# Performance work log

Measured on AMD Instinct MI355X. Metric: run time of the kernel, lower is better.

The kernel has to match this reference:

```python
import jax, jax.numpy as jnp
import numpy as np

EPS = 1e-6

def rms_norm(x):
    # RMSNorm over last dim, no learned weight (torch F.rms_norm without weight)
    return x * jax.lax.rsqrt(jnp.mean(jnp.square(x), axis=-1, keepdims=True) + EPS)

def apply_rotary_emb(x, cos, sin):
    # x: [b, t, h, d]; cos/sin: [t, d//2] -> broadcast [1, t, 1, d//2]
    half = x.shape[-1] // 2
    c = cos[None, :, None, :]
    s = sin[None, :, None, :]
    x1, x2 = x[..., :half], x[..., half:]
    return jnp.concatenate([x1 * c - x2 * s, x2 * c + x1 * s], axis=-1)

def setup_inputs() -> dict:
    key = jax.random.key(0)
    ks = jax.random.split(key, 16)
    B, T, E, H = 4, 2048, 1024, 16
    D = E // H
    inp = {
        "query": jax.random.normal(ks[0], (B, T, E), jnp.float32),
        "key": jax.random.normal(ks[1], (B, T, E), jnp.float32),
        "value": jax.random.normal(ks[2], (B, T, E), jnp.float32),
        "attn_mask": jnp.tril(jnp.ones((T, T), dtype=bool)),
        "cos": jnp.cos(jnp.arange(T)[:, None] / (10000.0 ** (jnp.arange(D // 2) / (D // 2)))[None, :]).astype(jnp.float32),
        "sin": jnp.sin(jnp.arange(T)[:, None] / (10000.0 ** (jnp.arange(D // 2) / (D // 2)))[None, :]).astype(jnp.float32),
        "Wq": jax.random.normal(ks[3], (E, E), jnp.float32) * 0.02,
        "bq": jnp.zeros((E,), jnp.float32),
        "Wk": jax.random.normal(ks[4], (E, E), jnp.float32) * 0.02,
        "bk": jnp.zeros((E,), jnp.float32),
        "Wv": jax.random.normal(ks[5], (E, E), jnp.float32) * 0.02,
        "bv": jnp.zeros((E,), jnp.float32),
        "Wo": jax.random.normal(ks[6], (E, E), jnp.float32) * 0.02,
        "bo": jnp.zeros((E,), jnp.float32),
    }
    return inp

def reference(query, key, value, attn_mask, cos, sin, Wq, bq, Wk, bk, Wv, bv, Wo, bo):
    B, T, E = query.shape
    H = 16
    D = E // H
    q = query @ Wq.T + bq
    k = key @ Wk.T + bk
    v = value @ Wv.T + bv
    q = q.reshape(B, T, H, D)
    k = k.reshape(B, T, H, D)
    v = v.reshape(B, T, H, D)
    q, k = rms_norm(q), rms_norm(k)
    q = apply_rotary_emb(q, cos, sin)
    k = apply_rotary_emb(k, cos, sin)
    # SDPA: [b, h, t, d] layout via einsum directly from [b, t, h, d]
    scale = 1.0 / jnp.sqrt(jnp.float32(D))
    scores = jnp.einsum('bqhd,bkhd->bhqk', q, k) * scale
    scores = jnp.where(attn_mask[None, None, :, :], scores, jnp.float32(-jnp.inf))
    attn = jax.nn.softmax(scores, axis=-1)
    o = jnp.einsum('bhqk,bkhd->bqhd', attn, v).reshape(B, T, E)
    return o @ Wo.T + bo
```

## Files before the change

### kernel.cpp

```cpp
#include <hip/hip_runtime.h>

typedef __bf16 bf16;
typedef __bf16 bf16x8 __attribute__((ext_vector_type(8)));
typedef __bf16 bf16x4 __attribute__((ext_vector_type(4)));
typedef float  floatx4 __attribute__((ext_vector_type(4)));

#define B_ 4
#define T_ 2048
#define E_ 1024
#define H_ 16
#define D_ 64
#define NTE_ (B_ * T_ * E_)

#define NEG_BIG (-1e30f)
#define SMAX2 12.2629081f

#define OFF_CQ 0ull
#define OFF_CK ((unsigned long long)NTE_)
#define OFF_CV (2ull * NTE_)
#define OFF_WQ (3ull * NTE_)
#define OFF_WK (OFF_WQ + 1048576ull)
#define OFF_WV (OFF_WK + 1048576ull)
#define OFF_WO (OFF_WV + 1048576ull)
__device__ bf16 g_conv[3ull * NTE_ + 4ull * 1048576ull];
__device__ bf16 g_scratch[5ull * NTE_];

__device__ __forceinline__ floatx4 mfma16(bf16x8 a, bf16x8 b, floatx4 c) {
  return __builtin_amdgcn_mfma_f32_16x16x32_bf16(a, b, c, 0, 0, 0);
}

__device__ __forceinline__ void async_copy16(void* lds, const void* g) {
  __builtin_amdgcn_global_load_lds(
      (const __attribute__((address_space(1))) unsigned int*)g,
      (__attribute__((address_space(3))) unsigned int*)lds, 16, 0, 0);
}

__global__ __launch_bounds__(256) void convert_all(const float4* __restrict__ q,
                                                   const float4* __restrict__ k,
                                                   const float4* __restrict__ v,
                                                   const float4* __restrict__ wq,
                                                   const float4* __restrict__ wk,
                                                   const float4* __restrict__ wv,
                                                   const float4* __restrict__ wo) {
  const float4* srcs[7] = {q, k, v, wq, wk, wv, wo};
  bf16x4* dsts[7] = {(bf16x4*)(g_conv + OFF_CQ), (bf16x4*)(g_conv + OFF_CK),
                     (bf16x4*)(g_conv + OFF_CV), (bf16x4*)(g_conv + OFF_WQ),
                     (bf16x4*)(g_conv + OFF_WK), (bf16x4*)(g_conv + OFF_WV),
                     (bf16x4*)(g_conv + OFF_WO)};
  const int n4s[7] = {NTE_ / 4, NTE_ / 4, NTE_ / 4, 262144, 262144, 262144, 262144};
  int i0 = blockIdx.x * 256 + threadIdx.x;
  int stride = gridDim.x * 256;
#pragma unroll
  for (int s = 0; s < 7; ++s) {
    const float4* sp = srcs[s];
    bf16x4* dp = dsts[s];
    int n4 = n4s[s];
    for (int i = i0; i < n4; i += stride) {
      float4 vv = sp[i];
      bf16x4 o;
      o[0] = (bf16)vv.x; o[1] = (bf16)vv.y; o[2] = (bf16)vv.z; o[3] = (bf16)vv.w;
      dp[i] = o;
    }
  }
}

template <int EPI>
__device__ __forceinline__ void gemm_core(char* __restrict__ smem,
                                          const bf16* __restrict__ X,
                                          const bf16* __restrict__ W,
                                          const float* __restrict__ bias,
                                          void* __restrict__ Yv, int M0, int N0,
                                          const float* __restrict__ cosb,
                                          const float* __restrict__ sinb) {
  constexpr int NT = 16;

  const int tid = threadIdx.x;
  const int w = tid >> 6;
  const int l = tid & 63;
  const int q = l >> 4;
  const int r = l & 15;
  const int lrow = l >> 3;
  const int rs7 = r & 7;
  const int wm = (w >> 2) * 64;
  const int wn = (w & 3) * 64;
  const int colb = ((l & 7) ^ lrow) << 4;
  const int sl0 = ((0 + q) ^ rs7) << 4;
  const int sl1 = ((4 + q) ^ rs7) << 4;

  char* const Ab = smem;
  char* const Bb = smem + 32768;
  const int aoff = (wm + r) * 128;
  const int boff = (wn + r) * 128;

  const char* gA = (const char*)X + (size_t)(M0 + w * 16 + lrow) * 2048 + colb;
  const char* gB = (const char*)W + (size_t)(N0 + w * 32 + lrow) * 2048 + colb;

  floatx4 acc[4][4];
#pragma unroll
  for (int mi = 0; mi < 4; ++mi)
#pragma unroll
    for (int ni = 0; ni < 4; ++ni) acc[mi][ni] = (floatx4){0.f, 0.f, 0.f, 0.f};

#define STA(p, t)                                              \
  do {                                                         \
    char* d_ = Ab + (p) * 16384 + w * 2048;                    \
    const char* s_ = gA + (size_t)(t) * 128;                   \
    async_copy16(d_, s_);                                      \
    async_copy16(d_ + 1024, s_ + 16384);                       \
  } while (0)
#define STB(p, t)                                              \
  do {                                                         \
    char* d_ = Bb + (p) * 32768 + w * 4096;                    \
    const char* s_ = gB + (size_t)(t) * 128;                   \
    async_copy16(d_, s_);                                      \
    async_copy16(d_ + 1024, s_ + 16384);                       \
    async_copy16(d_ + 2048, s_ + 32768);                       \
    async_copy16(d_ + 3072, s_ + 49152);                       \
  } while (0)

  STB(0, 0); STA(0, 0);
  STB(1, 1); STA(1, 1);
  asm volatile("s_waitcnt vmcnt(6)" ::: "memory");
  __builtin_amdgcn_s_barrier();

  bf16x8 af[4][2], bf0[2][2], bf1[2][2];

#pragma unroll 2
  for (int t = 0; t < NT; ++t) {
    const int p = t & 1;
    const char* rA = Ab + p * 16384;
    const char* rB = Bb + p * 32768;

#pragma unroll
    for (int mi = 0; mi < 4; ++mi) {
      af[mi][0] = *(const bf16x8*)(rA + aoff + mi * 2048 + sl0);
      af[mi][1] = *(const bf16x8*)(rA + aoff + mi * 2048 + sl1);
    }
#pragma unroll
    for (int ni = 0; ni < 2; ++ni) {
      bf0[ni][0] = *(const bf16x8*)(rB + boff + ni * 2048 + sl0);
      bf0[ni][1] = *(const bf16x8*)(rB + boff + ni * 2048 + sl1);
    }
    if (t >= 1 && t + 1 < NT) { STB(p ^ 1, t + 1); }
    __builtin_amdgcn_s_barrier();
    asm volatile("s_waitcnt lgkmcnt(0)" ::: "memory");
    __builtin_amdgcn_sched_barrier(0);
    __builtin_amdgcn_s_setprio(1);
#pragma unroll
    for (int mi = 0; mi < 4; ++mi)
#pragma unroll
      for (int ni = 0; ni < 2; ++ni) {
        acc[mi][ni] = mfma16(af[mi][0], bf0[ni][0], acc[mi][ni]);
        acc[mi][ni] = mfma16(af[mi][1], bf0[ni][1], acc[mi][ni]);
      }
    __builtin_amdgcn_s_setprio(0);
    __builtin_amdgcn_s_barrier();

#pragma unroll
    for (int ni = 0; ni < 2; ++ni) {
      bf1[ni][0] = *(const bf16x8*)(rB + boff + (ni + 2) * 2048 + sl0);
      bf1[ni][1] = *(const bf16x8*)(rB + boff + (ni + 2) * 2048 + sl1);
    }
    if (t + 2 < NT) { STA(p, t + 2); }
    __builtin_amdgcn_s_barrier();
    asm volatile("s_waitcnt lgkmcnt(0)" ::: "memory");
    __builtin_amdgcn_sched_barrier(0);
    __builtin_amdgcn_s_setprio(1);
#pragma unroll
    for (int mi = 0; mi < 4; ++mi)
#pragma unroll
      for (int ni = 0; ni < 2; ++ni) {
        acc[mi][ni + 2] = mfma16(af[mi][0], bf1[ni][0], acc[mi][ni + 2]);
        acc[mi][ni + 2] = mfma16(af[mi][1], bf1[ni][1], acc[mi][ni + 2]);
      }
    __builtin_amdgcn_s_setprio(0);
    if (t + 2 < NT) {
      asm volatile("s_waitcnt vmcnt(2)" ::: "memory");
    } else if (t + 1 < NT) {
      asm volatile("s_waitcnt vmcnt(0)" ::: "memory");
    }
    __builtin_amdgcn_s_barrier();
  }
#undef STA
#undef STB

  float bcol[4];
#pragma unroll
  for (int ni = 0; ni < 4; ++ni) bcol[ni] = bias[N0 + wn + ni * 16 + r];

  if (EPI == 0 || EPI == 1) {
    const float post = (EPI == 0) ? 0.18033688f : 1.0f;
    bf16* Y = (bf16*)Yv;
#pragma unroll
    for (int mi = 0; mi < 4; ++mi) {
      const int rowbase = M0 + wm + mi * 16 + q * 4;
#pragma unroll
      for (int rr = 0; rr < 4; ++rr) {
        const int row = rowbase + rr;
        const int ts = row & (T_ - 1);
        float v0 = acc[mi][0][rr] + bcol[0];
        float v1 = acc[mi][1][rr] + bcol[1];
        float v2 = acc[mi][2][rr] + bcol[2];
        float v3 = acc[mi][3][rr] + bcol[3];
        float ss = v0 * v0 + v1 * v1 + v2 * v2 + v3 * v3;
        ss += __shfl_xor(ss, 1, 64);
        ss += __shfl_xor(ss, 2, 64);
        ss += __shfl_xor(ss, 4, 64);
        ss += __shfl_xor(ss, 8, 64);
        const float rs = rsqrtf(ss * (1.0f / 64.0f) + 1e-6f);
        const float y0 = v0 * rs, y1 = v1 * rs, y2 = v2 * rs, y3 = v3 * rs;
        const float c0 = cosb[ts * 32 + r], s0 = sinb[ts * 32 + r];
        const float c1 = cosb[ts * 32 + 16 + r], s1 = sinb[ts * 32 + 16 + r];
        bf16 o0 = (bf16)((y0 * c0 - y2 * s0) * post);
        bf16 o1 = (bf16)((y1 * c1 - y3 * s1) * post);
        bf16 o2 = (bf16)((y2 * c0 + y0 * s0) * post);
        bf16 o3 = (bf16)((y3 * c1 + y1 * s1) * post);
        bf16* yp = Y + (size_t)row * 1024 + N0 + wn + r;
        yp[0] = o0; yp[16] = o1; yp[32] = o2; yp[48] = o3;
      }
    }
  } else if (EPI == 2) {
    bf16* Y = (bf16*)Yv;
#pragma unroll
    for (int mi = 0; mi < 4; ++mi) {
      const int rowbase = M0 + wm + mi * 16 + q * 4;
      const int bb = rowbase >> 11;
      const int t0 = rowbase & (T_ - 1);
#pragma unroll
      for (int ni = 0; ni < 4; ++ni) {
        const int col = N0 + wn + ni * 16 + r;
        const int head = col >> 6;
        const int d = col & 63;
        bf16x4 pk;
#pragma unroll
        for (int rr = 0; rr < 4; ++rr) pk[rr] = (bf16)(acc[mi][ni][rr] + bcol[ni]);
        *(bf16x4*)(Y + ((size_t)(bb * 16 + head) * 64 + d) * 2048 + t0) = pk;
      }
    }
  } else {
    float* Y = (float*)Yv;
#pragma unroll
    for (int mi = 0; mi < 4; ++mi) {
      const int rowbase = M0 + wm + mi * 16 + q * 4;
#pragma unroll
      for (int ni = 0; ni < 4; ++ni) {
        const int col = N0 + wn + ni * 16 + r;
#pragma unroll
        for (int rr = 0; rr < 4; ++rr)
          Y[(size_t)(rowbase + rr) * 1024 + col] = acc[mi][ni][rr] + bcol[ni];
      }
    }
  }
}

__global__ __launch_bounds__(512, 1) void gemm_qkv(const float* __restrict__ bq,
                                                   const float* __restrict__ bk,
                                                   const float* __restrict__ bv,
                                                   const float* __restrict__ cosb,
                                                   const float* __restrict__ sinb) {
  __shared__ __align__(16) char smem[98304];
  int bid = blockIdx.x;
  int s = (bid & 7) * 96 + (bid >> 3);
  int z = s >> 8;
  int rem = s & 255;
  int mt = rem >> 2, nt = rem & 3;
  const bf16* X = g_conv + OFF_CQ + (unsigned long long)z * NTE_;
  const bf16* W = g_conv + OFF_WQ + (unsigned long long)z * 1048576ull;
  if (z == 0) {
    gemm_core<0>(smem, X, W, bq, (void*)g_scratch, mt * 128, nt * 256, cosb, sinb);
  } else if (z == 1) {
    gemm_core<1>(smem, X, W, bk, (void*)(g_scratch + (unsigned long long)NTE_),
                 mt * 128, nt * 256, cosb, sinb);
  } else {
    gemm_core<2>(smem, X, W, bv, (void*)(g_scratch + 3ull * NTE_),
                 mt * 128, nt * 256, nullptr, nullptr);
  }
}

__global__ __launch_bounds__(512, 1) void gemm_out(const bf16* __restrict__ X,
                                                   const bf16* __restrict__ W,
                                                   const float* __restrict__ bias,
                                                   float* __restrict__ Y) {
  __shared__ __align__(16) char smem[98304];
  int bid = blockIdx.x;
  int s = (bid & 7) * 32 + (bid >> 3);
  int mt = s >> 2, nt = s & 3;
  gemm_core<3>(smem, X, W, bias, (void*)Y, mt * 128, nt * 256, nullptr, nullptr);
}

#define KSTR 72
#define PSTR 72
__global__ __launch_bounds__(256, 4) void flash_attn() {
  const bf16* qp = g_scratch;
  const bf16* kp = g_scratch + (unsigned long long)NTE_;
  const bf16* vt = g_scratch + 3ull * NTE_;
  bf16* op = g_scratch + 4ull * NTE_;

  __shared__ __align__(16) bf16 sK[64 * KSTR];
  __shared__ __align__(16) bf16 sV[64 * KSTR];
  __shared__ __align__(16) bf16 sP[4 * 32 * PSTR];

  const int bid = blockIdx.x;
  const int xcd = bid & 7;
  const int lb = bid >> 3;
  const int bh = xcd * 8 + (lb & 7);
  const int qt = 15 - (lb >> 3);
  const int h = bh & 15, b = bh >> 4;
  const int tid = threadIdx.x, w = tid >> 6, l = tid & 63, g = l >> 4, r = l & 15;
  const int Q0 = qt * 128;
  const int qw = Q0 + w * 32;

  const bf16* kbase = kp + (size_t)(b * T_) * E_ + h * D_;
  const bf16* vbase = vt + (size_t)bh * D_ * T_;
  bf16* pw = sP + w * (32 * PSTR);

  bf16x8 ones;
#pragma unroll
  for (int i = 0; i < 8; ++i) ones[i] = (bf16)1.0f;

  bf16x8 qa[2][2];
#pragma unroll
  for (int qb = 0; qb < 2; ++qb)
#pragma unroll
    for (int hf = 0; hf < 2; ++hf)
      qa[qb][hf] = *(const bf16x8*)(qp + (size_t)(b * T_ + qw + qb * 16 + r) * E_ +
                                    h * D_ + hf * 32 + g * 8);

  floatx4 o_acc[2][4], l_acc[2];
#pragma unroll
  for (int qb = 0; qb < 2; ++qb) {
    l_acc[qb] = (floatx4){0.f, 0.f, 0.f, 0.f};
#pragma unroll
    for (int dt = 0; dt < 4; ++dt) o_acc[qb][dt] = (floatx4){0.f, 0.f, 0.f, 0.f};
  }

  int srow[2], scc[2];
#pragma unroll
  for (int i = 0; i < 2; ++i) {
    int idx = i * 256 + tid;
    srow[i] = idx >> 3;
    scc[i] = (idx & 7) * 8;
  }

  bf16x8 kreg[2], vreg[2];
#pragma unroll
  for (int i = 0; i < 2; ++i) {
    kreg[i] = *(const bf16x8*)(kbase + (size_t)srow[i] * E_ + scc[i]);
    vreg[i] = *(const bf16x8*)(vbase + (size_t)srow[i] * T_ + scc[i]);
  }

  const int lastKt = Q0 + 64;
  for (int kt0 = 0; kt0 <= lastKt; kt0 += 64) {
    __syncthreads();
#pragma unroll
    for (int i = 0; i < 2; ++i) {
      *(bf16x8*)(sK + srow[i] * KSTR + scc[i]) = kreg[i];
      *(bf16x8*)(sV + srow[i] * KSTR + scc[i]) = vreg[i];
    }
    if (kt0 < lastKt) {
      int kt1 = kt0 + 64;
#pragma unroll
      for (int i = 0; i < 2; ++i) {
        kreg[i] = *(const bf16x8*)(kbase + (size_t)(kt1 + srow[i]) * E_ + scc[i]);
        vreg[i] = *(const bf16x8*)(vbase + (size_t)srow[i] * T_ + kt1 + scc[i]);
      }
    }
    __syncthreads();

    if (kt0 <= qw + 31) {
      const bool needMask = (kt0 + 63 > qw);

#pragma unroll
      for (int sc = 0; sc < 4; ++sc) {
        bf16x8 kb0 = *(const bf16x8*)(sK + (sc * 16 + r) * KSTR + g * 8);
        bf16x8 kb1 = *(const bf16x8*)(sK + (sc * 16 + r) * KSTR + 32 + g * 8);
        floatx4 s0 = (floatx4){0.f, 0.f, 0.f, 0.f};
        floatx4 s1 = (floatx4){0.f, 0.f, 0.f, 0.f};
        s0 = mfma16(kb0, qa[0][0], s0);
        s0 = mfma16(kb1, qa[0][1], s0);
        s1 = mfma16(kb0, qa[1][0], s1);
        s1 = mfma16(kb1, qa[1][1], s1);

        if (needMask) {
          int kg = kt0 + sc * 16 + g * 4;
          int qg0 = qw + r;
          int qg1 = qw + 16 + r;
#pragma unroll
          for (int rr = 0; rr < 4; ++rr) {
            if (kg + rr > qg0) s0[rr] = NEG_BIG;
            if (kg + rr > qg1) s1[rr] = NEG_BIG;
          }
        }

        bf16x4 p0, p1;
#pragma unroll
        for (int rr = 0; rr < 4; ++rr) {
          p0[rr] = (bf16)exp2f(s0[rr] - SMAX2);
          p1[rr] = (bf16)exp2f(s1[rr] - SMAX2);
        }
        *(bf16x4*)(pw + r * PSTR + sc * 16 + g * 4) = p0;
        *(bf16x4*)(pw + (16 + r) * PSTR + sc * 16 + g * 4) = p1;
      }

#pragma unroll
      for (int kk = 0; kk < 2; ++kk) {
        bf16x8 vb[4];
#pragma unroll
        for (int dt = 0; dt < 4; ++dt)
          vb[dt] = *(const bf16x8*)(sV + (dt * 16 + r) * KSTR + kk * 32 + g * 8);
#pragma unroll
        for (int qb = 0; qb < 2; ++qb) {
          bf16x8 pa = *(const bf16x8*)(pw + (qb * 16 + r) * PSTR + kk * 32 + g * 8);
          l_acc[qb] = mfma16(pa, ones, l_acc[qb]);
#pragma unroll
          for (int dt = 0; dt < 4; ++dt)
            o_acc[qb][dt] = mfma16(pa, vb[dt], o_acc[qb][dt]);
        }
      }
    }
  }

  float linv[2][4];
#pragma unroll
  for (int qb = 0; qb < 2; ++qb)
#pragma unroll
    for (int rr = 0; rr < 4; ++rr) linv[qb][rr] = 1.0f / l_acc[qb][rr];
#pragma unroll
  for (int qb = 0; qb < 2; ++qb)
#pragma unroll
    for (int dt = 0; dt < 4; ++dt)
#pragma unroll
      for (int rr = 0; rr < 4; ++rr) {
        int t = qw + qb * 16 + g * 4 + rr;
        op[(size_t)(b * T_ + t) * E_ + h * D_ + dt * 16 + r] =
            (bf16)(o_acc[qb][dt][rr] * linv[qb][rr]);
      }
}

extern "C" void kernel_launch(void* const* d_in, const int* in_sizes, int n_in,
                              void* d_out, int out_size, void* d_ws, size_t ws_size,
                              hipStream_t stream) {
  float* out = (float*)d_out;

  void* cvp_ = nullptr;
  void* sp_ = nullptr;
  (void)hipGetSymbolAddress(&cvp_, HIP_SYMBOL(g_conv));
  (void)hipGetSymbolAddress(&sp_, HIP_SYMBOL(g_scratch));
  bf16* cv = (bf16*)cvp_;
  bf16* sc = (bf16*)sp_;

  const float* cosb = (const float*)d_in[4];
  const float* sinb = (const float*)d_in[5];
  const float* bq = (const float*)d_in[7];
  const float* bk = (const float*)d_in[9];
  const float* bv = (const float*)d_in[11];
  const float* bo = (const float*)d_in[13];

  convert_all<<<dim3(1024), dim3(256), 0, stream>>>(
      (const float4*)d_in[0], (const float4*)d_in[1], (const float4*)d_in[2],
      (const float4*)d_in[6], (const float4*)d_in[8], (const float4*)d_in[10],
      (const float4*)d_in[12]);

  bf16* op = sc + 4ull * NTE_;

  gemm_qkv<<<dim3(768), dim3(512), 0, stream>>>(bq, bk, bv, cosb, sinb);
  flash_attn<<<dim3(1024), dim3(256), 0, stream>>>();
  gemm_out<<<dim3(256), dim3(512), 0, stream>>>(op, cv + OFF_WO, bo, out);
}
```

Before: 327.6 us.

## Triple-buffer GEMM LDS pipeline with a single barrier per K-step

Restructures the shared GEMM core used by the QKV and output projections. It replaces the double-buffered, two-half-step schedule with a three-stage LDS ring, prefetched two tiles ahead. Each K-iteration now loads all B fragments at once, issues 32 MFMAs, and synchronises with one barrier instead of several. The aim is to hide global-load latency better and cut barrier and waitcnt stalls. In exchange, LDS use per block rises to 144 KB, the setprio/sched_barrier interleaving is dropped, and full unrolling raises register pressure.

```diff
diff --git a/kernel.cpp b/kernel.cpp
--- a/kernel.cpp
+++ b/kernel.cpp
@@ -88,7 +88,7 @@
   const int sl1 = ((4 + q) ^ rs7) << 4;
 
   char* const Ab = smem;
-  char* const Bb = smem + 32768;
+  char* const Bb = smem + 49152;
   const int aoff = (wm + r) * 128;
   const int boff = (wn + r) * 128;
 
@@ -101,16 +101,16 @@
 #pragma unroll
     for (int ni = 0; ni < 4; ++ni) acc[mi][ni] = (floatx4){0.f, 0.f, 0.f, 0.f};
 
-#define STA(p, t)                                              \
+#define STA(bi, t)                                             \
   do {                                                         \
-    char* d_ = Ab + (p) * 16384 + w * 2048;                    \
+    char* d_ = Ab + (bi) * 16384 + w * 2048;                   \
     const char* s_ = gA + (size_t)(t) * 128;                   \
     async_copy16(d_, s_);                                      \
     async_copy16(d_ + 1024, s_ + 16384);                       \
   } while (0)
-#define STB(p, t)                                              \
+#define STB(bi, t)                                             \
   do {                                                         \
-    char* d_ = Bb + (p) * 32768 + w * 4096;                    \
+    char* d_ = Bb + (bi) * 32768 + w * 4096;                   \
     const char* s_ = gB + (size_t)(t) * 128;                   \
     async_copy16(d_, s_);                                      \
     async_copy16(d_ + 1024, s_ + 16384);                       \
@@ -120,66 +120,45 @@
 
   STB(0, 0); STA(0, 0);
   STB(1, 1); STA(1, 1);
-  asm volatile("s_waitcnt vmcnt(6)" ::: "memory");
-  __builtin_amdgcn_s_barrier();
-
-  bf16x8 af[4][2], bf0[2][2], bf1[2][2];
-
-#pragma unroll 2
+  STB(2, 2); STA(2, 2);
+  asm volatile("s_waitcnt vmcnt(12)" ::: "memory");
+  asm volatile("s_barrier" ::: "memory");
+
+#pragma unroll
   for (int t = 0; t < NT; ++t) {
-    const int p = t & 1;
-    const char* rA = Ab + p * 16384;
-    const char* rB = Bb + p * 32768;
-
+    const int ib = t % 3;
+    const int st = (t + 2) % 3;
+
+    if (t >= 1 && t + 2 < NT) { STB(st, t + 2); STA(st, t + 2); }
+
+    const char* rA = Ab + ib * 16384;
+    const char* rB = Bb + ib * 32768;
+
+    bf16x8 af[4][2], bv[4][2];
 #pragma unroll
     for (int mi = 0; mi < 4; ++mi) {
       af[mi][0] = *(const bf16x8*)(rA + aoff + mi * 2048 + sl0);
       af[mi][1] = *(const bf16x8*)(rA + aoff + mi * 2048 + sl1);
     }
 #pragma unroll
-    for (int ni = 0; ni < 2; ++ni) {
-      bf0[ni][0] = *(const bf16x8*)(rB + boff + ni * 2048 + sl0);
-      bf0[ni][1] = *(const bf16x8*)(rB + boff + ni * 2048 + sl1);
-    }
-    if (t >= 1 && t + 1 < NT) { STB(p ^ 1, t + 1); }
-    __builtin_amdgcn_s_barrier();
-    asm volatile("s_waitcnt lgkmcnt(0)" ::: "memory");
-    __builtin_amdgcn_sched_barrier(0);
-    __builtin_amdgcn_s_setprio(1);
+    for (int ni = 0; ni < 4; ++ni) {
+      bv[ni][0] = *(const bf16x8*)(rB + boff + ni * 2048 + sl0);
+      bv[ni][1] = *(const bf16x8*)(rB + boff + ni * 2048 + sl1);
+    }
 #pragma unroll
     for (int mi = 0; mi < 4; ++mi)
 #pragma unroll
-      for (int ni = 0; ni < 2; ++ni) {
-        acc[mi][ni] = mfma16(af[mi][0], bf0[ni][0], acc[mi][ni]);
-        acc[mi][ni] = mfma16(af[mi][1], bf0[ni][1], acc[mi][ni]);
-      }
-    __builtin_amdgcn_s_setprio(0);
-    __builtin_amdgcn_s_barrier();
-
-#pragma unroll
-    for (int ni = 0; ni < 2; ++ni) {
-      bf1[ni][0] = *(const bf16x8*)(rB + boff + (ni + 2) * 2048 + sl0);
-      bf1[ni][1] = *(const bf16x8*)(rB + boff + (ni + 2) * 2048 + sl1);
-    }
-    if (t + 2 < NT) { STA(p, t + 2); }
-    __builtin_amdgcn_s_barrier();
-    asm volatile("s_waitcnt lgkmcnt(0)" ::: "memory");
-    __builtin_amdgcn_sched_barrier(0);
-    __builtin_amdgcn_s_setprio(1);
-#pragma unroll
-    for (int mi = 0; mi < 4; ++mi)
-#pragma unroll
-      for (int ni = 0; ni < 2; ++ni) {
-        acc[mi][ni + 2] = mfma16(af[mi][0], bf1[ni][0], acc[mi][ni + 2]);
-        acc[mi][ni + 2] = mfma16(af[mi][1], bf1[ni][1], acc[mi][ni + 2]);
-      }
-    __builtin_amdgcn_s_setprio(0);
-    if (t + 2 < NT) {
-      asm volatile("s_waitcnt vmcnt(2)" ::: "memory");
-    } else if (t + 1 < NT) {
+      for (int ni = 0; ni < 4; ++ni) {
+        acc[mi][ni] = mfma16(af[mi][0], bv[ni][0], acc[mi][ni]);
+        acc[mi][ni] = mfma16(af[mi][1], bv[ni][1], acc[mi][ni]);
+      }
+
+    if (t + 3 <= NT) {
+      asm volatile("s_waitcnt vmcnt(6)" ::: "memory");
+    } else if (t + 2 == NT) {
       asm volatile("s_waitcnt vmcnt(0)" ::: "memory");
     }
-    __builtin_amdgcn_s_barrier();
+    if (t + 1 < NT) asm volatile("s_barrier" ::: "memory");
   }
 #undef STA
 #undef STB
@@ -258,7 +237,7 @@
                                                    const float* __restrict__ bv,
                                                    const float* __restrict__ cosb,
                                                    const float* __restrict__ sinb) {
-  __shared__ __align__(16) char smem[98304];
+  __shared__ __align__(16) char smem[147456];
   int bid = blockIdx.x;
   int s = (bid & 7) * 96 + (bid >> 3);
   int z = s >> 8;
@@ -281,7 +260,7 @@
                                                    const bf16* __restrict__ W,
                                                    const float* __restrict__ bias,
                                                    float* __restrict__ Y) {
-  __shared__ __align__(16) char smem[98304];
+  __shared__ __align__(16) char smem[147456];
   int bid = blockIdx.x;
   int s = (bid & 7) * 32 + (bid >> 3);
   int mt = s >> 2, nt = s & 3;
```

Result: no change. 324.1 us (-1.1%).

## Use triple-buffered GEMM pipeline for output projection; trim barriers in QKV GEMM

Applied to the files above, without the earlier changes.

Splits the shared GEMM core into two variants. The QKV variant drops two intra-iteration barriers so loads and MFMAs interleave with less synchronisation. The output-projection variant switches to a 3-stage shared-memory ring (144KB LDS), issuing loads two tiles ahead and doing all 32 MFMAs per k-step with one barrier, to hide global latency on the small 256-block grid. This trades more LDS and a race risk: the removed barriers may allow the next STB to overwrite a buffer that other waves are still reading.

```diff
diff --git a/kernel.cpp b/kernel.cpp
--- a/kernel.cpp
+++ b/kernel.cpp
@@ -65,125 +65,12 @@
 }
 
 template <int EPI>
-__device__ __forceinline__ void gemm_core(char* __restrict__ smem,
-                                          const bf16* __restrict__ X,
-                                          const bf16* __restrict__ W,
-                                          const float* __restrict__ bias,
-                                          void* __restrict__ Yv, int M0, int N0,
-                                          const float* __restrict__ cosb,
-                                          const float* __restrict__ sinb) {
-  constexpr int NT = 16;
-
-  const int tid = threadIdx.x;
-  const int w = tid >> 6;
-  const int l = tid & 63;
-  const int q = l >> 4;
-  const int r = l & 15;
-  const int lrow = l >> 3;
-  const int rs7 = r & 7;
-  const int wm = (w >> 2) * 64;
-  const int wn = (w & 3) * 64;
-  const int colb = ((l & 7) ^ lrow) << 4;
-  const int sl0 = ((0 + q) ^ rs7) << 4;
-  const int sl1 = ((4 + q) ^ rs7) << 4;
-
-  char* const Ab = smem;
-  char* const Bb = smem + 32768;
-  const int aoff = (wm + r) * 128;
-  const int boff = (wn + r) * 128;
-
-  const char* gA = (const char*)X + (size_t)(M0 + w * 16 + lrow) * 2048 + colb;
-  const char* gB = (const char*)W + (size_t)(N0 + w * 32 + lrow) * 2048 + colb;
-
-  floatx4 acc[4][4];
-#pragma unroll
-  for (int mi = 0; mi < 4; ++mi)
-#pragma unroll
-    for (int ni = 0; ni < 4; ++ni) acc[mi][ni] = (floatx4){0.f, 0.f, 0.f, 0.f};
-
-#define STA(p, t)                                              \
-  do {                                                         \
-    char* d_ = Ab + (p) * 16384 + w * 2048;                    \
-    const char* s_ = gA + (size_t)(t) * 128;                   \
-    async_copy16(d_, s_);                                      \
-    async_copy16(d_ + 1024, s_ + 16384);                       \
-  } while (0)
-#define STB(p, t)                                              \
-  do {                                                         \
-    char* d_ = Bb + (p) * 32768 + w * 4096;                    \
-    const char* s_ = gB + (size_t)(t) * 128;                   \
-    async_copy16(d_, s_);                                      \
-    async_copy16(d_ + 1024, s_ + 16384);                       \
-    async_copy16(d_ + 2048, s_ + 32768);                       \
-    async_copy16(d_ + 3072, s_ + 49152);                       \
-  } while (0)
-
-  STB(0, 0); STA(0, 0);
-  STB(1, 1); STA(1, 1);
-  asm volatile("s_waitcnt vmcnt(6)" ::: "memory");
-  __builtin_amdgcn_s_barrier();
-
-  bf16x8 af[4][2], bf0[2][2], bf1[2][2];
-
-#pragma unroll 2
-  for (int t = 0; t < NT; ++t) {
-    const int p = t & 1;
-    const char* rA = Ab + p * 16384;
-    const char* rB = Bb + p * 32768;
-
-#pragma unroll
-    for (int mi = 0; mi < 4; ++mi) {
-      af[mi][0] = *(const bf16x8*)(rA + aoff + mi * 2048 + sl0);
-      af[mi][1] = *(const bf16x8*)(rA + aoff + mi * 2048 + sl1);
-    }
-#pragma unroll
-    for (int ni = 0; ni < 2; ++ni) {
-      bf0[ni][0] = *(const bf16x8*)(rB + boff + ni * 2048 + sl0);
-      bf0[ni][1] = *(const bf16x8*)(rB + boff + ni * 2048 + sl1);
-    }
-    if (t >= 1 && t + 1 < NT) { STB(p ^ 1, t + 1); }
-    __builtin_amdgcn_s_barrier();
-    asm volatile("s_waitcnt lgkmcnt(0)" ::: "memory");
-    __builtin_amdgcn_sched_barrier(0);
-    __builtin_amdgcn_s_setprio(1);
-#pragma unroll
-    for (int mi = 0; mi < 4; ++mi)
-#pragma unroll
-      for (int ni = 0; ni < 2; ++ni) {
-        acc[mi][ni] = mfma16(af[mi][0], bf0[ni][0], acc[mi][ni]);
-        acc[mi][ni] = mfma16(af[mi][1], bf0[ni][1], acc[mi][ni]);
-      }
-    __builtin_amdgcn_s_setprio(0);
-    __builtin_amdgcn_s_barrier();
-
-#pragma unroll
-    for (int ni = 0; ni < 2; ++ni) {
-      bf1[ni][0] = *(const bf16x8*)(rB + boff + (ni + 2) * 2048 + sl0);
-      bf1[ni][1] = *(const bf16x8*)(rB + boff + (ni + 2) * 2048 + sl1);
-    }
-    if (t + 2 < NT) { STA(p, t + 2); }
-    __builtin_amdgcn_s_barrier();
-    asm volatile("s_waitcnt lgkmcnt(0)" ::: "memory");
-    __builtin_amdgcn_sched_barrier(0);
-    __builtin_amdgcn_s_setprio(1);
-#pragma unroll
-    for (int mi = 0; mi < 4; ++mi)
-#pragma unroll
-      for (int ni = 0; ni < 2; ++ni) {
-        acc[mi][ni + 2] = mfma16(af[mi][0], bf1[ni][0], acc[mi][ni + 2]);
-        acc[mi][ni + 2] = mfma16(af[mi][1], bf1[ni][1], acc[mi][ni + 2]);
-      }
-    __builtin_amdgcn_s_setprio(0);
-    if (t + 2 < NT) {
-      asm volatile("s_waitcnt vmcnt(2)" ::: "memory");
-    } else if (t + 1 < NT) {
-      asm volatile("s_waitcnt vmcnt(0)" ::: "memory");
-    }
-    __builtin_amdgcn_s_barrier();
-  }
-#undef STA
-#undef STB
-
+__device__ __forceinline__ void gemm_epilogue(floatx4 (&acc)[4][4],
+                                              const float* __restrict__ bias,
+                                              void* __restrict__ Yv, int M0, int N0,
+                                              int wm, int wn, int q, int r,
+                                              const float* __restrict__ cosb,
+                                              const float* __restrict__ sinb) {
   float bcol[4];
 #pragma unroll
   for (int ni = 0; ni < 4; ++ni) bcol[ni] = bias[N0 + wn + ni * 16 + r];
@@ -253,6 +140,229 @@
   }
 }
 
+template <int EPI>
+__device__ __forceinline__ void gemm_coreA(char* __restrict__ smem,
+                                           const bf16* __restrict__ X,
+                                           const bf16* __restrict__ W,
+                                           const float* __restrict__ bias,
+                                           void* __restrict__ Yv, int M0, int N0,
+                                           const float* __restrict__ cosb,
+                                           const float* __restrict__ sinb) {
+  constexpr int NT = 16;
+
+  const int tid = threadIdx.x;
+  const int w = tid >> 6;
+  const int l = tid & 63;
+  const int q = l >> 4;
+  const int r = l & 15;
+  const int lrow = l >> 3;
+  const int rs7 = r & 7;
+  const int wm = (w >> 2) * 64;
+  const int wn = (w & 3) * 64;
+  const int colb = ((l & 7) ^ lrow) << 4;
+  const int sl0 = ((0 + q) ^ rs7) << 4;
+  const int sl1 = ((4 + q) ^ rs7) << 4;
+
+  char* const Ab = smem;
+  char* const Bb = smem + 32768;
+  const int aoff = (wm + r) * 128;
+  const int boff = (wn + r) * 128;
+
+  const char* gA = (const char*)X + (size_t)(M0 + w * 16 + lrow) * 2048 + colb;
+  const char* gB = (const char*)W + (size_t)(N0 + w * 32 + lrow) * 2048 + colb;
+
+  floatx4 acc[4][4];
+#pragma unroll
+  for (int mi = 0; mi < 4; ++mi)
+#pragma unroll
+    for (int ni = 0; ni < 4; ++ni) acc[mi][ni] = (floatx4){0.f, 0.f, 0.f, 0.f};
+
+#define STA(p, t)                                              \
+  do {                                                         \
+    char* d_ = Ab + (p) * 16384 + w * 2048;                    \
+    const char* s_ = gA + (size_t)(t) * 128;                   \
+    async_copy16(d_, s_);                                      \
+    async_copy16(d_ + 1024, s_ + 16384);                       \
+  } while (0)
+#define STB(p, t)                                              \
+  do {                                                         \
+    char* d_ = Bb + (p) * 32768 + w * 4096;                    \
+    const char* s_ = gB + (size_t)(t) * 128;                   \
+    async_copy16(d_, s_);                                      \
+    async_copy16(d_ + 1024, s_ + 16384);                       \
+    async_copy16(d_ + 2048, s_ + 32768);                       \
+    async_copy16(d_ + 3072, s_ + 49152);                       \
+  } while (0)
+
+  STB(0, 0); STA(0, 0);
+  STB(1, 1); STA(1, 1);
+  asm volatile("s_waitcnt vmcnt(6)" ::: "memory");
+  __builtin_amdgcn_s_barrier();
+
+  bf16x8 af[4][2], bf0[2][2], bf1[2][2];
+
+#pragma unroll 2
+  for (int t = 0; t < NT; ++t) {
+    const int p = t & 1;
+    const char* rA = Ab + p * 16384;
+    const char* rB = Bb + p * 32768;
+
+#pragma unroll
+    for (int mi = 0; mi < 4; ++mi) {
+      af[mi][0] = *(const bf16x8*)(rA + aoff + mi * 2048 + sl0);
+      af[mi][1] = *(const bf16x8*)(rA + aoff + mi * 2048 + sl1);
+    }
+#pragma unroll
+    for (int ni = 0; ni < 2; ++ni) {
+      bf0[ni][0] = *(const bf16x8*)(rB + boff + ni * 2048 + sl0);
+      bf0[ni][1] = *(const bf16x8*)(rB + boff + ni * 2048 + sl1);
+    }
+    if (t >= 1 && t + 1 < NT) { STB(p ^ 1, t + 1); }
+    asm volatile("s_waitcnt lgkmcnt(0)" ::: "memory");
+    __builtin_amdgcn_sched_barrier(0);
+    __builtin_amdgcn_s_setprio(1);
+#pragma unroll
+    for (int mi = 0; mi < 4; ++mi)
+#pragma unroll
+      for (int ni = 0; ni < 2; ++ni) {
+        acc[mi][ni] = mfma16(af[mi][0], bf0[ni][0], acc[mi][ni]);
+        acc[mi][ni] = mfma16(af[mi][1], bf0[ni][1], acc[mi][ni]);
+      }
+    __builtin_amdgcn_s_setprio(0);
+    __builtin_amdgcn_s_barrier();
+
+#pragma unroll
+    for (int ni = 0; ni < 2; ++ni) {
+      bf1[ni][0] = *(const bf16x8*)(rB + boff + (ni + 2) * 2048 + sl0);
+      bf1[ni][1] = *(const bf16x8*)(rB + boff + (ni + 2) * 2048 + sl1);
+    }
+    if (t + 2 < NT) { STA(p, t + 2); }
+    asm volatile("s_waitcnt lgkmcnt(0)" ::: "memory");
+    __builtin_amdgcn_sched_barrier(0);
+    __builtin_amdgcn_s_setprio(1);
+#pragma unroll
+    for (int mi = 0; mi < 4; ++mi)
+#pragma unroll
+      for (int ni = 0; ni < 2; ++ni) {
+        acc[mi][ni + 2] = mfma16(af[mi][0], bf1[ni][0], acc[mi][ni + 2]);
+        acc[mi][ni + 2] = mfma16(af[mi][1], bf1[ni][1], acc[mi][ni + 2]);
+      }
+    __builtin_amdgcn_s_setprio(0);
+    if (t + 2 < NT) {
+      asm volatile("s_waitcnt vmcnt(2)" ::: "memory");
+    } else if (t + 1 < NT) {
+      asm volatile("s_waitcnt vmcnt(0)" ::: "memory");
+    }
+    __builtin_amdgcn_s_barrier();
+  }
+#undef STA
+#undef STB
+
+  gemm_epilogue<EPI>(acc, bias, Yv, M0, N0, wm, wn, q, r, cosb, sinb);
+}
+
+template <int EPI>
+__device__ __forceinline__ void gemm_coreB(char* __restrict__ smem,
+                                           const bf16* __restrict__ X,
+                                           const bf16* __restrict__ W,
+                                           const float* __restrict__ bias,
+                                           void* __restrict__ Yv, int M0, int N0,
+                                           const float* __restrict__ cosb,
+                                           const float* __restrict__ sinb) {
+  constexpr int NT = 16;
+
+  const int tid = threadIdx.x;
+  const int w = tid >> 6;
+  const int l = tid & 63;
+  const int q = l >> 4;
+  const int r = l & 15;
+  const int lrow = l >> 3;
+  const int rs7 = r & 7;
+  const int wm = (w >> 2) * 64;
+  const int wn = (w & 3) * 64;
+  const int colb = ((l & 7) ^ lrow) << 4;
+  const int sl0 = ((0 + q) ^ rs7) << 4;
+  const int sl1 = ((4 + q) ^ rs7) << 4;
+
+  char* const Ab = smem;
+  char* const Bb = smem + 49152;
+  const int aoff = (wm + r) * 128;
+  const int boff = (wn + r) * 128;
+
+  const char* gA = (const char*)X + (size_t)(M0 + w * 16 + lrow) * 2048 + colb;
+  const char* gB = (const char*)W + (size_t)(N0 + w * 32 + lrow) * 2048 + colb;
+
+  floatx4 acc[4][4];
+#pragma unroll
+  for (int mi = 0; mi < 4; ++mi)
+#pragma unroll
+    for (int ni = 0; ni < 4; ++ni) acc[mi][ni] = (floatx4){0.f, 0.f, 0.f, 0.f};
+
+#define STA(bi, t)                                             \
+  do {                                                         \
+    char* d_ = Ab + (bi) * 16384 + w * 2048;                   \
+    const char* s_ = gA + (size_t)(t) * 128;                   \
+    async_copy16(d_, s_);                                      \
+    async_copy16(d_ + 1024, s_ + 16384);                       \
+  } while (0)
+#define STB(bi, t)                                             \
+  do {                                                         \
+    char* d_ = Bb + (bi) * 32768 + w * 4096;                   \
+    const char* s_ = gB + (size_t)(t) * 128;                   \
+    async_copy16(d_, s_);                                      \
+    async_copy16(d_ + 1024, s_ + 16384);                       \
+    async_copy16(d_ + 2048, s_ + 32768);                       \
+    async_copy16(d_ + 3072, s_ + 49152);                       \
+  } while (0)
+
+  STB(0, 0); STA(0, 0);
+  STB(1, 1); STA(1, 1);
+  STB(2, 2); STA(2, 2);
+  asm volatile("s_waitcnt vmcnt(12)" ::: "memory");
+  asm volatile("s_barrier" ::: "memory");
+
+#pragma unroll
+  for (int t = 0; t < NT; ++t) {
+    const int ib = t % 3;
+    const int st = (t + 2) % 3;
+
+    if (t >= 1 && t + 2 < NT) { STB(st, t + 2); STA(st, t + 2); }
+
+    const char* rA = Ab + ib * 16384;
+    const char* rB = Bb + ib * 32768;
+
+    bf16x8 af[4][2], bv[4][2];
+#pragma unroll
+    for (int mi = 0; mi < 4; ++mi) {
+      af[mi][0] = *(const bf16x8*)(rA + aoff + mi * 2048 + sl0);
+      af[mi][1] = *(const bf16x8*)(rA + aoff + mi * 2048 + sl1);
+    }
+#pragma unroll
+    for (int ni = 0; ni < 4; ++ni) {
+      bv[ni][0] = *(const bf16x8*)(rB + boff + ni * 2048 + sl0);
+      bv[ni][1] = *(const bf16x8*)(rB + boff + ni * 2048 + sl1);
+    }
+#pragma unroll
+    for (int mi = 0; mi < 4; ++mi)
+#pragma unroll
+      for (int ni = 0; ni < 4; ++ni) {
+        acc[mi][ni] = mfma16(af[mi][0], bv[ni][0], acc[mi][ni]);
+        acc[mi][ni] = mfma16(af[mi][1], bv[ni][1], acc[mi][ni]);
+      }
+
+    if (t + 3 <= NT) {
+      asm volatile("s_waitcnt vmcnt(6)" ::: "memory");
+    } else if (t + 2 == NT) {
+      asm volatile("s_waitcnt vmcnt(0)" ::: "memory");
+    }
+    if (t + 1 < NT) asm volatile("s_barrier" ::: "memory");
+  }
+#undef STA
+#undef STB
+
+  gemm_epilogue<EPI>(acc, bias, Yv, M0, N0, wm, wn, q, r, cosb, sinb);
+}
+
 __global__ __launch_bounds__(512, 1) void gemm_qkv(const float* __restrict__ bq,
                                                    const float* __restrict__ bk,
                                                    const float* __restrict__ bv,
@@ -267,13 +377,13 @@
   const bf16* X = g_conv + OFF_CQ + (unsigned long long)z * NTE_;
   const bf16* W = g_conv + OFF_WQ + (unsigned long long)z * 1048576ull;
   if (z == 0) {
-    gemm_core<0>(smem, X, W, bq, (void*)g_scratch, mt * 128, nt * 256, cosb, sinb);
+    gemm_coreA<0>(smem, X, W, bq, (void*)g_scratch, mt * 128, nt * 256, cosb, sinb);
   } else if (z == 1) {
-    gemm_core<1>(smem, X, W, bk, (void*)(g_scratch + (unsigned long long)NTE_),
-                 mt * 128, nt * 256, cosb, sinb);
+    gemm_coreA<1>(smem, X, W, bk, (void*)(g_scratch + (unsigned long long)NTE_),
+                  mt * 128, nt * 256, cosb, sinb);
   } else {
-    gemm_core<2>(smem, X, W, bv, (void*)(g_scratch + 3ull * NTE_),
-                 mt * 128, nt * 256, nullptr, nullptr);
+    gemm_coreA<2>(smem, X, W, bv, (void*)(g_scratch + 3ull * NTE_),
+                  mt * 128, nt * 256, nullptr, nullptr);
   }
 }
 
@@ -281,11 +391,11 @@
                                                    const bf16* __restrict__ W,
                                                    const float* __restrict__ bias,
                                                    float* __restrict__ Y) {
-  __shared__ __align__(16) char smem[98304];
+  __shared__ __align__(16) char smem[147456];
   int bid = blockIdx.x;
   int s = (bid & 7) * 32 + (bid >> 3);
   int mt = s >> 2, nt = s & 3;
-  gemm_core<3>(smem, X, W, bias, (void*)Y, mt * 128, nt * 256, nullptr, nullptr);
+  gemm_coreB<3>(smem, X, W, bias, (void*)Y, mt * 128, nt * 256, nullptr, nullptr);
 }
 
 #define KSTR 72
```

New measurement: 331.0 us. No clear change (+1.1%).
